# Kernel optimization log

Hardware: AMD Instinct MI355X
Metric: run time of the kernel (lower is better)

The kernel has to match this reference:

```python
import jax, jax.numpy as jnp
import numpy as np

B, S, L, C, H, W_IMG = 4, 2, 1024, 128, 256, 256
HEADS1, D1 = 4, C // 4          # layer 1: 4 heads x 32 dims, concat
HEADS2, D2 = 1, C               # layer 2: 1 head x 128 dims, mean
LN_EPS = 1e-5
NEG_SLOPE = 0.2


def _xavier(k, shape):
    limit = float(np.sqrt(6.0 / (shape[0] + shape[1])))
    return jax.random.uniform(k, shape, jnp.float32, -limit, limit)


def setup_inputs() -> dict:
    key = jax.random.key(0)
    ks = jax.random.split(key, 10)
    seg_feats = jax.random.normal(ks[0], (B, S, L, C), jnp.float32)
    # integer segment labels in 0..L (0 = background), stored per forward spec
    seg_images = jax.random.randint(ks[1], (B, S, H, W_IMG), 0, L + 1, jnp.int32)
    seg_nums = jnp.full((B, S), L, jnp.int32)
    return {
        "seg_feats": seg_feats,
        "seg_images": seg_images,
        "seg_nums": seg_nums,
        "W1": _xavier(ks[2], (HEADS1 * D1, C)),   # Linear weight (out, in)
        "a_src1": _xavier(ks[3], (HEADS1, D1)),
        "a_dst1": _xavier(ks[4], (HEADS1, D1)),
        "W2": _xavier(ks[5], (HEADS2 * D2, C)),
        "a_src2": _xavier(ks[6], (HEADS2, D2)),
        "a_dst2": _xavier(ks[7], (HEADS2, D2)),
        "ln_gamma": jnp.ones((C,), jnp.float32),
        "ln_beta": jnp.zeros((C,), jnp.float32),
    }


def build_adjacency(seg):
    """seg: (H, W) int labels in 1..L (0 = background) -> (L, L) float adj with self-loops."""
    adj = jnp.eye(L, dtype=jnp.float32)

    def add_edges(adj, a, b):
        valid = (a > 0) & (b > 0) & (a != b)
        ai = jnp.clip(a - 1, 0, L - 1)
        bi = jnp.clip(b - 1, 0, L - 1)
        v = valid.astype(jnp.float32)
        adj = adj.at[ai, bi].max(v)
        return adj.at[bi, ai].max(v)

    pairs = [
        (seg[:, :-1], seg[:, 1:]),       # horizontal
        (seg[:-1, :], seg[1:, :]),       # vertical
        (seg[:-1, :-1], seg[1:, 1:]),    # diagonal \
        (seg[:-1, 1:], seg[1:, :-1]),    # diagonal /
    ]
    for a, b in pairs:
        adj = add_edges(adj, a.reshape(-1), b.reshape(-1))
    return adj


def _leaky_relu(x):
    return jnp.where(x >= 0, x, NEG_SLOPE * x)


def gat_layer(x, adj, W, a_src, a_dst, heads, d, concat):
    N = x.shape[0]
    Wf = (x @ W.T).reshape(N, heads, d)                     # (N, h, d)
    e_src = jnp.einsum('nhd,hd->nh', Wf, a_src)             # (N, h)
    e_dst = jnp.einsum('nhd,hd->nh', Wf, a_dst)             # (N, h)
    e = _leaky_relu(e_src[:, None, :] + e_dst[None, :, :])  # (N, N, h)
    e = jnp.where((adj == 0)[:, :, None], -jnp.inf, e)
    alpha = jax.nn.softmax(e, axis=1)                       # softmax over neighbours j
    h = jnp.einsum('ijh,jhd->ihd', alpha, Wf)               # (N, h, d)
    if concat:
        return jax.nn.elu(h.reshape(N, heads * d))
    return h.mean(axis=1)


def reference(seg_feats, seg_images, seg_nums, W1, a_src1, a_dst1,
              W2, a_src2, a_dst2, ln_gamma, ln_beta):
    feats = seg_feats.reshape(B * S, L, C)
    adjs = jax.vmap(build_adjacency)(seg_images.reshape(B * S, H, W_IMG))

    def enrich(f, adj):
        h = gat_layer(f, adj, W1, a_src1, a_dst1, HEADS1, D1, True)
        h = gat_layer(h, adj, W2, a_src2, a_dst2, HEADS2, D2, False)
        y = f + h
        mu = jnp.mean(y, axis=-1, keepdims=True)
        var = jnp.var(y, axis=-1, keepdims=True)
        return (y - mu) * jax.lax.rsqrt(var + LN_EPS) * ln_gamma + ln_beta

    out = jax.vmap(enrich)(feats, adjs)
    return out.reshape(B, S, L, C)
```

## Files before the change

kernel.cpp:

```cpp
#include <hip/hip_runtime.h>
#include <hip/hip_bf16.h>
#include <stdint.h>

#define LL 1024
#define CC 128
#define NG 8
#define NN (NG*LL)
typedef __hip_bfloat16 bf16;
typedef __attribute__((ext_vector_type(8))) short short8;
typedef __attribute__((ext_vector_type(4))) short short4v;
typedef __attribute__((ext_vector_type(4))) float f32x4;

__device__ __forceinline__ bool is_bf16_wire(const void* gamma) {
  return *(const uint32_t*)gamma == 0x3F803F80u;
}
__device__ __forceinline__ float ldw(const void* p, size_t i, bool bf) {
  return bf ? __bfloat162float(((const bf16*)p)[i]) : ((const float*)p)[i];
}
__device__ __forceinline__ uint32_t encf(float f) {
  uint32_t b = __float_as_uint(f);
  return (b & 0x80000000u) ? ~b : (b | 0x80000000u);
}
__device__ __forceinline__ float decf(uint32_t u) {
  return (u & 0x80000000u) ? __uint_as_float(u & 0x7FFFFFFFu) : __uint_as_float(~u);
}
__device__ __forceinline__ short f2bs(float x) {
  uint32_t u = __float_as_uint(x);
  u += 0x7FFFu + ((u >> 16) & 1u);
  return (short)(u >> 16);
}
template <bool BFW>
__device__ __forceinline__ short8 ld8w(const void* p, size_t off) {
  if (BFW) {
    return *(const short8*)((const bf16*)p + off);
  } else {
    const float4* f = (const float4*)((const float*)p + off);
    float4 a = f[0], b = f[1];
    short8 r;
    r[0] = f2bs(a.x); r[1] = f2bs(a.y); r[2] = f2bs(a.z); r[3] = f2bs(a.w);
    r[4] = f2bs(b.x); r[5] = f2bs(b.y); r[6] = f2bs(b.z); r[7] = f2bs(b.w);
    return r;
  }
}


template <int NH, bool BFW>
__device__ __forceinline__ void gemm_core(const short8 af[4],
    const void* __restrict__ Wsrc, const void* __restrict__ as_,
    const void* __restrict__ ad_, bf16* __restrict__ WfT,
    float* __restrict__ es, float* __restrict__ ed,
    uint32_t* __restrict__ edmax, int n0, int lane) {
  int quad = lane >> 4, c = lane & 15;
  int g = n0 >> 10;
  f32x4 acc[8];
#pragma unroll
  for (int dt = 0; dt < 8; dt++) acc[dt] = (f32x4){0.f, 0.f, 0.f, 0.f};
#pragma unroll
  for (int ks = 0; ks < 4; ks++)
#pragma unroll
    for (int dt = 0; dt < 8; dt++) {
      short8 bfr = ld8w<BFW>(Wsrc, (size_t)(dt * 16 + c) * CC + ks * 32 + quad * 8);
      acc[dt] = __builtin_amdgcn_mfma_f32_16x16x32_bf16(af[ks], bfr, acc[dt], 0, 0, 0);
    }
  {
    int nw4 = ((n0 & 1023) >> 2) + quad;
    bf16* wdst = WfT + (size_t)g * 131072 + (size_t)nw4 * 512 + c * 4;
#pragma unroll
    for (int dt = 0; dt < 8; dt++) {
      short4v pk;
#pragma unroll
      for (int r = 0; r < 4; r++) pk[r] = f2bs(acc[dt][r]);
      *(short4v*)&wdst[dt * 64] = pk;
    }
  }
  float sv[NH][4], dv[NH][4];
#pragma unroll
  for (int h = 0; h < NH; h++)
#pragma unroll
    for (int r = 0; r < 4; r++) { sv[h][r] = 0.f; dv[h][r] = 0.f; }
#pragma unroll
  for (int dt = 0; dt < 8; dt++) {
    int o = dt * 16 + c;
    float a_s = ldw(as_, o, BFW);
    float a_d = ldw(ad_, o, BFW);
    int h = (NH == 4) ? (dt >> 1) : 0;
#pragma unroll
    for (int r = 0; r < 4; r++) {
      sv[h][r] += acc[dt][r] * a_s;
      dv[h][r] += acc[dt][r] * a_d;
    }
  }
#pragma unroll
  for (int m = 1; m <= 8; m <<= 1)
#pragma unroll
    for (int h = 0; h < NH; h++)
#pragma unroll
      for (int r = 0; r < 4; r++) {
        sv[h][r] += __shfl_xor(sv[h][r], m);
        dv[h][r] += __shfl_xor(dv[h][r], m);
      }
  if (c == 0) {
#pragma unroll
    for (int r = 0; r < 4; r++) {
      int node = n0 + quad * 4 + r;
#pragma unroll
      for (int h = 0; h < NH; h++) {
        es[node * NH + h] = sv[h][r];
        ed[node * NH + h] = dv[h][r];
      }
    }
  }
  float mq[NH];
#pragma unroll
  for (int h = 0; h < NH; h++) {
    mq[h] = fmaxf(fmaxf(dv[h][0], dv[h][1]), fmaxf(dv[h][2], dv[h][3]));
    mq[h] = fmaxf(mq[h], __shfl_xor(mq[h], 16));
    mq[h] = fmaxf(mq[h], __shfl_xor(mq[h], 32));
  }
  if (lane == 0)
#pragma unroll
    for (int h = 0; h < NH; h++)
      atomicMax(&edmax[g * NH + h], encf(mq[h]));
}

template <bool BFW>
__device__ __forceinline__ void gemm1_body(const void* __restrict__ feats,
    const void* __restrict__ W1, const void* __restrict__ as1,
    const void* __restrict__ ad1, bf16* __restrict__ WfT,
    float* __restrict__ es, float* __restrict__ ed,
    uint32_t* __restrict__ edmax, int bb, int t) {
  int lane = t & 63, w = t >> 6;
  int quad = lane >> 4, c = lane & 15;
  int n0 = bb * 64 + w * 16;
  short8 af[4];
#pragma unroll
  for (int ks = 0; ks < 4; ks++)
    af[ks] = ld8w<BFW>(feats, (size_t)(n0 + c) * CC + ks * 32 + quad * 8);
  gemm_core<4, BFW>(af, W1, as1, ad1, WfT, es, ed, edmax, n0, lane);
}

__global__ __launch_bounds__(256) void k_front(
    const void* __restrict__ feats, const void* __restrict__ W1,
    const void* __restrict__ as1, const void* __restrict__ ad1,
    const void* __restrict__ gamma, const int* __restrict__ img,
    uint8_t* __restrict__ adj, bf16* __restrict__ WfT,
    float* __restrict__ es, float* __restrict__ ed,
    uint32_t* __restrict__ edmax) {
  int bid = blockIdx.x;
  if (bid < 2048) {
    int g = bid & 7;
    int y = bid >> 3;
    int x = threadIdx.x;
    int p = y * 256 + x;
    const int* im = img + g * 65536;
    uint8_t* A = adj + ((size_t)g << 20);
    int a = im[p];
    if (a > 0) {
      int nxs[4] = {x + 1, x, x + 1, x - 1};
      int nys[4] = {y, y + 1, y + 1, y + 1};
#pragma unroll
      for (int d = 0; d < 4; d++) {
        int nx = nxs[d], ny = nys[d];
        if (nx < 0 || nx > 255 || ny > 255) continue;
        int b = im[ny * 256 + nx];
        if (b > 0 && b != a) {
          A[(size_t)(a - 1) * LL + (b - 1)] = 1;
          A[(size_t)(b - 1) * LL + (a - 1)] = 1;
        }
      }
    }
  } else {
    int bb = bid - 2048;
    if (is_bf16_wire(gamma))
      gemm1_body<true>(feats, W1, as1, ad1, WfT, es, ed, edmax, bb, threadIdx.x);
    else
      gemm1_body<false>(feats, W1, as1, ad1, WfT, es, ed, edmax, bb, threadIdx.x);
  }
}

template <int NH>
__global__ __launch_bounds__(256) void k_attn(
    const bf16* __restrict__ WfT, const float* __restrict__ esb,
    const float* __restrict__ edb, const uint8_t* __restrict__ adjb,
    const uint32_t* __restrict__ edmax, bf16* __restrict__ pacc,
    float* __restrict__ pml) {
  __shared__ __align__(16) float red[4224];
  __shared__ float eds[NH * 520];
  __shared__ float lred[4][16 * NH];
  int t = threadIdx.x;
  int lane = t & 63, w = t >> 6;
  int quad = lane >> 4, c = lane & 15;
  int bid = blockIdx.x;
  int jp = bid & 1, rt = (bid >> 1) & 63, g = bid >> 7;
  int i0 = rt * 16;
  int node = g * LL + i0 + c;
  int J0 = jp * 512 + w * 128;
  for (int u = t; u < 512 * NH; u += 256) {
    int h = u >> 9, j = u & 511;
    eds[h * 520 + j] = edb[(size_t)(g * LL + jp * 512 + j) * NH + h];
  }
  const float LOG2E = 1.44269504f;
  float esv[NH], cmv[NH];
  if (NH == 4) {
    const float4 e4 = *(const float4*)&esb[(size_t)node * 4];
    esv[0] = e4.x; esv[1] = e4.y; esv[2] = e4.z; esv[3] = e4.w;
  } else {
    esv[0] = esb[node];
  }
#pragma unroll
  for (int h = 0; h < NH; h++) {
    float mx = decf(edmax[NH == 4 ? g * 4 + h : g]);
    float m = esv[h] + mx; m = fmaxf(m, 0.2f * m);
    cmv[h] = -m * LOG2E;
  }
  int rowg = i0 + c;
  const uint8_t* arow = adjb + ((size_t)g << 20) + (size_t)rowg * 1024 + jp * 512 + w * 128;
  uint2 mbj[4];
#pragma unroll
  for (int jb = 0; jb < 4; jb++)
    mbj[jb] = *(const uint2*)&arow[jb * 32 + quad * 8];
  f32x4 acc[8];
#pragma unroll
  for (int dt = 0; dt < 8; dt++) acc[dt] = (f32x4){0.f, 0.f, 0.f, 0.f};
  float lsum[NH];
#pragma unroll
  for (int h = 0; h < NH; h++) lsum[h] = 0.f;
  const bf16* wb = WfT + (size_t)g * 131072 + (size_t)J0 * 128 + quad * 1024 + c * 4;
  __syncthreads();

  union FB { uint2 u[2]; short8 s; };
#pragma unroll
  for (int jb = 0; jb < 4; jb++) {
    short8 frag[8];
#pragma unroll
    for (int dt = 0; dt < 8; dt++) {
      FB f;
      f.u[0] = *(const uint2*)&wb[jb * 4096 + dt * 64];
      f.u[1] = *(const uint2*)&wb[jb * 4096 + dt * 64 + 512];
      frag[dt] = f.s;
    }
    int base_wj = w * 128 + jb * 32 + quad * 8;
    int jg0 = jp * 512 + base_wj;
    uint32_t bx = mbj[jb].x, by = mbj[jb].y;
    float mf[8];
#pragma unroll
    for (int i = 0; i < 8; i++) {
      uint32_t bit = (i < 4) ? ((bx >> (8 * i)) & 1u) : ((by >> (8 * (i - 4))) & 1u);
      mf[i] = (float)(bit | (uint32_t)(jg0 + i == rowg));
    }
#pragma unroll
    for (int h = 0; h < NH; h++) {
      const float* ep = &eds[h * 520 + base_wj];
      float4 ea = *(const float4*)ep;
      float4 eb = *(const float4*)(ep + 4);
      float ev[8] = {ea.x, ea.y, ea.z, ea.w, eb.x, eb.y, eb.z, eb.w};
      float pr[8];
      float lac = 0.f;
#pragma unroll
      for (int i = 0; i < 8; i++) {
        float e = esv[h] + ev[i];
        e = fmaxf(e, 0.2f * e);
        float p = exp2f(fmaf(e, LOG2E, cmv[h]));
        p *= mf[i];
        lac += p;
        pr[i] = p;
      }
      lsum[h] += lac;
      union { short8 s; uint32_t u[4]; } A;
#pragma unroll
      for (int k = 0; k < 4; k++) {
        __hip_bfloat162 q = __float22bfloat162_rn(make_float2(pr[2*k], pr[2*k+1]));
        A.u[k] = *reinterpret_cast<uint32_t*>(&q);
      }
#pragma unroll
      for (int d2 = 0; d2 < 8 / NH; d2++) {
        int dt = h * (8 / NH) + d2;
        acc[dt] = __builtin_amdgcn_mfma_f32_16x16x32_bf16(A.s, frag[dt], acc[dt], 0, 0, 0);
      }
    }
  }
#pragma unroll
  for (int h = 0; h < NH; h++) {
    float v = lsum[h];
    v += __shfl_xor(v, 16);
    v += __shfl_xor(v, 32);
    lsum[h] = v;
  }
  if (quad == 0)
#pragma unroll
    for (int h = 0; h < NH; h++) lred[w][c * NH + h] = lsum[h];
  if (w == 1)
#pragma unroll
    for (int dt = 0; dt < 8; dt++) *(f32x4*)&red[dt * 256 + lane * 4] = acc[dt];
  if (w == 3)
#pragma unroll
    for (int dt = 0; dt < 8; dt++) *(f32x4*)&red[2048 + dt * 256 + lane * 4] = acc[dt];
  __syncthreads();
  if (w == 0)
#pragma unroll
    for (int dt = 0; dt < 8; dt++) acc[dt] += *(const f32x4*)&red[dt * 256 + lane * 4];
  if (w == 2)
#pragma unroll
    for (int dt = 0; dt < 8; dt++) acc[dt] += *(const f32x4*)&red[2048 + dt * 256 + lane * 4];
  __syncthreads();
  if (w == 2)
#pragma unroll
    for (int dt = 0; dt < 8; dt++) *(f32x4*)&red[dt * 256 + lane * 4] = acc[dt];
  __syncthreads();
  if (w == 0) {
#pragma unroll
    for (int dt = 0; dt < 8; dt++) acc[dt] += *(const f32x4*)&red[dt * 256 + lane * 4];
#pragma unroll
    for (int dt = 0; dt < 8; dt++)
#pragma unroll
      for (int r = 0; r < 4; r++)
        red[2048 + (quad * 4 + r) * 132 + dt * 16 + c] = acc[dt][r];
  }
  __syncthreads();
  {
    int row = t >> 4, d0 = (t & 15) * 8;
    const float* src = &red[2048 + row * 132 + d0];
    short8 pk;
#pragma unroll
    for (int k = 0; k < 8; k++) pk[k] = f2bs(src[k]);
    *(short8*)&pacc[((size_t)jp * NN + g * LL + i0 + row) * CC + d0] = pk;
  }
  if (t < 16 * NH) {
    float l = lred[0][t] + lred[1][t] + lred[2][t] + lred[3][t];
    int row = (NH == 4) ? (t >> 2) : t;
    int h = (NH == 4) ? (t & 3) : 0;
    if (NH == 4) pml[((size_t)jp * NN + g * LL + i0 + row) * 4 + h] = l;
    else         pml[(size_t)jp * NN + g * LL + i0 + row] = l;
  }
}

template <bool BFW>
__device__ __forceinline__ void gemm2_body(const bf16* __restrict__ pacc,
    const float* __restrict__ pml1, const void* __restrict__ W2,
    const void* __restrict__ as2, const void* __restrict__ ad2,
    bf16* __restrict__ WfT, float* __restrict__ es, float* __restrict__ ed,
    uint32_t* __restrict__ edmax, int bid, int t) {
  int lane = t & 63, w = t >> 6;
  int quad = lane >> 4, c = lane & 15;
  int n0 = bid * 64 + w * 16;
  int node = n0 + c;
  float4 l4 = make_float4(0.f, 0.f, 0.f, 0.f);
#pragma unroll
  for (int p = 0; p < 2; p++) {
    float4 v = *(const float4*)&pml1[((size_t)p * NN + node) * 4];
    l4.x += v.x; l4.y += v.y; l4.z += v.z; l4.w += v.w;
  }
  float linv[4] = {1.f / l4.x, 1.f / l4.y, 1.f / l4.z, 1.f / l4.w};
  short8 af[4];
#pragma unroll
  for (int ks = 0; ks < 4; ks++) {
    float a[8] = {0.f, 0.f, 0.f, 0.f, 0.f, 0.f, 0.f, 0.f};
#pragma unroll
    for (int p = 0; p < 2; p++) {
      short8 v = *(const short8*)&pacc[((size_t)p * NN + node) * CC + ks * 32 + quad * 8];
#pragma unroll
      for (int i = 0; i < 8; i++) {
        union { short s[2]; float f; } cv; cv.s[0] = 0; cv.s[1] = v[i];
        a[i] += cv.f;
      }
    }
#pragma unroll
    for (int i = 0; i < 8; i++) {
      float vv = a[i] * linv[ks];
      vv = (vv > 0.f) ? vv : (__expf(vv) - 1.f);
      af[ks][i] = f2bs(vv);
    }
  }
  gemm_core<1, BFW>(af, W2, as2, ad2, WfT, es, ed, edmax, n0, lane);
}

__global__ __launch_bounds__(256) void k_gemm2c(
    const bf16* __restrict__ pacc, const float* __restrict__ pml1,
    const void* __restrict__ W2, const void* __restrict__ as2,
    const void* __restrict__ ad2, const void* __restrict__ gamma,
    bf16* __restrict__ WfT, float* __restrict__ es, float* __restrict__ ed,
    uint32_t* __restrict__ edmax) {
  if (is_bf16_wire(gamma))
    gemm2_body<true>(pacc, pml1, W2, as2, ad2, WfT, es, ed, edmax, blockIdx.x, threadIdx.x);
  else
    gemm2_body<false>(pacc, pml1, W2, as2, ad2, WfT, es, ed, edmax, blockIdx.x, threadIdx.x);
}

__global__ __launch_bounds__(256) void k_combine2(const bf16* __restrict__ pacc,
    const float* __restrict__ pml2, const void* __restrict__ feats,
    const void* __restrict__ gamma, const void* __restrict__ beta,
    void* __restrict__ outp) {
  const bool bf = is_bf16_wire(gamma);
  int t = threadIdx.x;
  int node = blockIdx.x * 4 + (t >> 6);
  int lane = t & 63;
  float l = 0.f, a0 = 0.f, a1 = 0.f;
#pragma unroll
  for (int p = 0; p < 2; p++) {
    l  += pml2[(size_t)p * NN + node];
    a0 += __bfloat162float(pacc[((size_t)p * NN + node) * CC + lane]);
    a1 += __bfloat162float(pacc[((size_t)p * NN + node) * CC + 64 + lane]);
  }
  float y0 = ldw(feats, (size_t)node * CC + lane, bf) + a0 / l;
  float y1 = ldw(feats, (size_t)node * CC + 64 + lane, bf) + a1 / l;
  float s = y0 + y1, s2 = y0 * y0 + y1 * y1;
#pragma unroll
  for (int mm = 32; mm >= 1; mm >>= 1) { s += __shfl_xor(s, mm); s2 += __shfl_xor(s2, mm); }
  float mu = s * (1.f / 128.f);
  float var = fmaxf(s2 * (1.f / 128.f) - mu * mu, 0.f);
  float rs = rsqrtf(var + 1e-5f);
  float o0 = (y0 - mu) * rs * ldw(gamma, lane, bf) + ldw(beta, lane, bf);
  float o1 = (y1 - mu) * rs * ldw(gamma, 64 + lane, bf) + ldw(beta, 64 + lane, bf);
  if (bf) {
    ((bf16*)outp)[(size_t)node * CC + lane]      = __float2bfloat16(o0);
    ((bf16*)outp)[(size_t)node * CC + 64 + lane] = __float2bfloat16(o1);
  } else {
    ((float*)outp)[(size_t)node * CC + lane]      = o0;
    ((float*)outp)[(size_t)node * CC + 64 + lane] = o1;
  }
}

extern "C" void kernel_launch(void* const* d_in, const int* in_sizes, int n_in,
                              void* d_out, int out_size, void* d_ws, size_t ws_size,
                              hipStream_t stream) {
  const void* feats = d_in[0];
  const int*  imgs  = (const int*)d_in[1];
  const void* W1    = d_in[3];
  const void* as1   = d_in[4];
  const void* ad1   = d_in[5];
  const void* W2    = d_in[6];
  const void* as2   = d_in[7];
  const void* ad2   = d_in[8];
  const void* gamma = d_in[9];
  const void* beta  = d_in[10];

  char* ws = (char*)d_ws;
  uint8_t*  adj    = (uint8_t*)ws;
  uint32_t* edmax1 = (uint32_t*)(ws + 8388608);
  uint32_t* edmax2 = (uint32_t*)(ws + 8388736);
  bf16*     WfT    = (bf16*)(ws + 8519680);
  float*    es1    = (float*)(ws + 10616832);
  float*    ed1    = (float*)(ws + 10747904);
  float*    es2    = (float*)(ws + 10878976);
  float*    ed2    = (float*)(ws + 10911744);
  float*    pml    = (float*)(ws + 10944512);
  bf16*     pacc   = (bf16*)(ws + 11206656);

  hipMemsetAsync(ws, 0, 8389120, stream);
  hipLaunchKernelGGL(k_front, dim3(2176), dim3(256), 0, stream,
                     feats, W1, as1, ad1, gamma, imgs,
                     adj, WfT, es1, ed1, edmax1);
  hipLaunchKernelGGL((k_attn<4>), dim3(1024), dim3(256), 0, stream,
                     WfT, es1, ed1, adj, edmax1, pacc, pml);
  hipLaunchKernelGGL(k_gemm2c, dim3(128), dim3(256), 0, stream,
                     pacc, pml, W2, as2, ad2, gamma, WfT, es2, ed2, edmax2);
  hipLaunchKernelGGL((k_attn<1>), dim3(1024), dim3(256), 0, stream,
                     WfT, es2, ed2, adj, edmax2, pacc, pml);
  hipLaunchKernelGGL(k_combine2, dim3(2048), dim3(256), 0, stream,
                     pacc, pml, feats, gamma, beta, d_out);
}
```

Baseline: 186.0 us.

## Write one-sided adjacency, symmetrize in attention via shared column tile, interleave graphs

The adjacency builder now writes only the (a,b) edge direction. The attention kernel recovers the symmetric mask by staging the transposed column slice of the adjacency into shared memory and OR-ing it with the row bits. This halves the scattered byte stores in the front kernel, at the cost of an extra 8 KB strided read and a shared-memory lookup per mask element in attention. Block-to-node mappings are also changed so consecutive blocks cycle across the 8 graphs, and the GEMM blocks are moved ahead of the adjacency blocks in the front kernel, presumably to spread work and memory traffic.

New measurement: 179.0 us. -3.8%, faster.

```diff
diff --git a/kernel.cpp b/kernel.cpp
--- a/kernel.cpp
+++ b/kernel.cpp
@@ -131,7 +131,7 @@
     uint32_t* __restrict__ edmax, int bb, int t) {
   int lane = t & 63, w = t >> 6;
   int quad = lane >> 4, c = lane & 15;
-  int n0 = bb * 64 + w * 16;
+  int n0 = (bb & 7) * 1024 + (bb >> 3) * 64 + w * 16;
   short8 af[4];
 #pragma unroll
   for (int ks = 0; ks < 4; ks++)
@@ -147,34 +147,33 @@
     float* __restrict__ es, float* __restrict__ ed,
     uint32_t* __restrict__ edmax) {
   int bid = blockIdx.x;
-  if (bid < 2048) {
-    int g = bid & 7;
-    int y = bid >> 3;
-    int x = threadIdx.x;
-    int p = y * 256 + x;
-    const int* im = img + g * 65536;
-    uint8_t* A = adj + ((size_t)g << 20);
-    int a = im[p];
-    if (a > 0) {
-      int nxs[4] = {x + 1, x, x + 1, x - 1};
-      int nys[4] = {y, y + 1, y + 1, y + 1};
-#pragma unroll
-      for (int d = 0; d < 4; d++) {
-        int nx = nxs[d], ny = nys[d];
-        if (nx < 0 || nx > 255 || ny > 255) continue;
-        int b = im[ny * 256 + nx];
-        if (b > 0 && b != a) {
-          A[(size_t)(a - 1) * LL + (b - 1)] = 1;
-          A[(size_t)(b - 1) * LL + (a - 1)] = 1;
-        }
-      }
-    }
-  } else {
-    int bb = bid - 2048;
+  if (bid < 128) {
     if (is_bf16_wire(gamma))
-      gemm1_body<true>(feats, W1, as1, ad1, WfT, es, ed, edmax, bb, threadIdx.x);
+      gemm1_body<true>(feats, W1, as1, ad1, WfT, es, ed, edmax, bid, threadIdx.x);
     else
-      gemm1_body<false>(feats, W1, as1, ad1, WfT, es, ed, edmax, bb, threadIdx.x);
+      gemm1_body<false>(feats, W1, as1, ad1, WfT, es, ed, edmax, bid, threadIdx.x);
+    return;
+  }
+  int rel = bid - 128;
+  int g = rel & 7;
+  int y = rel >> 3;
+  int x = threadIdx.x;
+  int p = y * 256 + x;
+  const int* im = img + g * 65536;
+  uint8_t* A = adj + ((size_t)g << 20);
+  int a = im[p];
+  if (a > 0) {
+    int nxs[4] = {x + 1, x, x + 1, x - 1};
+    int nys[4] = {y, y + 1, y + 1, y + 1};
+#pragma unroll
+    for (int d = 0; d < 4; d++) {
+      int nx = nxs[d], ny = nys[d];
+      if (nx < 0 || nx > 255 || ny > 255) continue;
+      int b = im[ny * 256 + nx];
+      if (b > 0 && b != a) {
+        A[(size_t)(a - 1) * LL + (b - 1)] = 1;
+      }
+    }
   }
 }
 
@@ -187,17 +186,24 @@
   __shared__ __align__(16) float red[4224];
   __shared__ float eds[NH * 520];
   __shared__ float lred[4][16 * NH];
+  __shared__ uint8_t scol[512 * 20];
   int t = threadIdx.x;
   int lane = t & 63, w = t >> 6;
   int quad = lane >> 4, c = lane & 15;
   int bid = blockIdx.x;
-  int jp = bid & 1, rt = (bid >> 1) & 63, g = bid >> 7;
+  int g = bid & 7, jp = (bid >> 3) & 1, rt = bid >> 4;
   int i0 = rt * 16;
   int node = g * LL + i0 + c;
   int J0 = jp * 512 + w * 128;
   for (int u = t; u < 512 * NH; u += 256) {
     int h = u >> 9, j = u & 511;
     eds[h * 520 + j] = edb[(size_t)(g * LL + jp * 512 + j) * NH + h];
+  }
+  for (int u = t; u < 512; u += 256) {
+    const uint8_t* src = adjb + ((size_t)g << 20) + (size_t)(jp * 512 + u) * 1024 + i0;
+    uint4 v = *(const uint4*)src;
+    uint32_t* dst = (uint32_t*)&scol[u * 20];
+    dst[0] = v.x; dst[1] = v.y; dst[2] = v.z; dst[3] = v.w;
   }
   const float LOG2E = 1.44269504f;
   float esv[NH], cmv[NH];
@@ -246,7 +252,9 @@
 #pragma unroll
     for (int i = 0; i < 8; i++) {
       uint32_t bit = (i < 4) ? ((bx >> (8 * i)) & 1u) : ((by >> (8 * (i - 4))) & 1u);
-      mf[i] = (float)(bit | (uint32_t)(jg0 + i == rowg));
+      uint32_t cb = scol[(base_wj + i) * 20 + c];
+      uint32_t mm = bit | cb | (uint32_t)(jg0 + i == rowg);
+      mf[i] = (float)(mm != 0u);
     }
 #pragma unroll
     for (int h = 0; h < NH; h++) {
@@ -342,7 +350,7 @@
     uint32_t* __restrict__ edmax, int bid, int t) {
   int lane = t & 63, w = t >> 6;
   int quad = lane >> 4, c = lane & 15;
-  int n0 = bid * 64 + w * 16;
+  int n0 = (bid & 7) * 1024 + (bid >> 3) * 64 + w * 16;
   int node = n0 + c;
   float4 l4 = make_float4(0.f, 0.f, 0.f, 0.f);
 #pragma unroll
@@ -392,7 +400,7 @@
     void* __restrict__ outp) {
   const bool bf = is_bf16_wire(gamma);
   int t = threadIdx.x;
-  int node = blockIdx.x * 4 + (t >> 6);
+  int node = (blockIdx.x & 7) * 1024 + (blockIdx.x >> 3) * 4 + (t >> 6);
   int lane = t & 63;
   float l = 0.f, a0 = 0.f, a1 = 0.f;
 #pragma unroll
```
